# Performance work log

Hardware: AMD Instinct MI355X
Metric: run time of the kernel (lower is better)

Reference implementation:

```python
import jax, jax.numpy as jnp
import numpy as np

OBS, ACT, EMB, HID, NQ = 512, 32, 512, 512, 32
B = 32768


def setup_inputs() -> dict:
    key = jax.random.key(0)
    ks = jax.random.split(key, 12)
    s_in = 1.0 / np.sqrt(OBS + ACT)
    s_emb = 1.0 / np.sqrt(EMB)
    s_hid = 1.0 / np.sqrt(HID)
    return {
        "observation": jax.random.normal(ks[0], (B, OBS), jnp.float32),
        "prev_action": jax.random.normal(ks[1], (B, ACT), jnp.float32),
        "hidden_state": jax.random.normal(ks[2], (HID,), jnp.float32),
        "cell_state": jax.random.normal(ks[3], (HID,), jnp.float32),
        "W1": jax.random.uniform(ks[4], (EMB, OBS + ACT), jnp.float32, -s_in, s_in),
        "b1": jax.random.uniform(ks[5], (EMB,), jnp.float32, -s_in, s_in),
        "W_ih": jax.random.uniform(ks[6], (4 * HID, EMB), jnp.float32, -s_hid, s_hid),
        "b_ih": jax.random.uniform(ks[7], (4 * HID,), jnp.float32, -s_hid, s_hid),
        "W_hh": jax.random.uniform(ks[8], (4 * HID, HID), jnp.float32, -s_hid, s_hid),
        "b_hh": jax.random.uniform(ks[9], (4 * HID,), jnp.float32, -s_hid, s_hid),
        "W2": jax.random.uniform(ks[10], (NQ, HID), jnp.float32, -s_hid, s_hid),
        "b2": jax.random.uniform(ks[11], (NQ,), jnp.float32, -s_hid, s_hid),
    }


def reference(observation, prev_action, hidden_state, cell_state,
              W1, b1, W_ih, b_ih, W_hh, b_hh, W2, b2):
    # MLP1: Linear + ReLU over concat(obs, prev_action)  -> [B, EMB]
    x = jnp.concatenate([observation, prev_action], axis=-1)
    x = jax.nn.relu(x @ W1.T + b1)

    # Original torch code loops LSTMCell over batch, but reuses the SAME
    # (hidden_state, cell_state) every iteration -> fully batchable.
    # gates: [B, 4H]; h contribution is identical for all rows (broadcast).
    gates = x @ W_ih.T + b_ih + (hidden_state @ W_hh.T + b_hh)
    i, f, g, o = jnp.split(gates, 4, axis=-1)  # torch LSTMCell gate order
    i = jax.nn.sigmoid(i)
    f = jax.nn.sigmoid(f)
    g = jnp.tanh(g)
    o = jax.nn.sigmoid(o)
    c_new = f * cell_state + i * g          # [B, HID]
    h_new = o * jnp.tanh(c_new)             # [B, HID]

    q_values = h_new @ W2.T + b2             # [B, NQ]
    # torch returns last loop iteration's (h, c)
    return q_values, h_new[-1], c_new[-1]
```

## Files before the change

kernel.cpp:

```cpp
#include <hip/hip_runtime.h>
#include <stdint.h>

#define DEVINL __device__ __forceinline__

typedef __attribute__((ext_vector_type(8))) __bf16 bf16x8;
typedef __attribute__((ext_vector_type(4))) float f32x4;
typedef __attribute__((ext_vector_type(16))) float f32x16;
typedef __attribute__((ext_vector_type(4))) int i32x4;
typedef __attribute__((ext_vector_type(8))) int i32x8;

DEVINL unsigned short f2bf(float f) {
  union { float f; unsigned int u; } v; v.f = f;
  unsigned int u = v.u;
  return (unsigned short)((u + 0x7fffu + ((u >> 16) & 1u)) >> 16);
}

DEVINL unsigned char f2fp8(float f) {
  return (unsigned char)(__builtin_amdgcn_cvt_pk_fp8_f32(f, f, 0, false) & 0xff);
}

DEVINL float sigm(float x) { return __builtin_amdgcn_rcpf(1.f + __expf(-x)); }
DEVINL float tanh_(float x) {
  return 1.f - 2.f * __builtin_amdgcn_rcpf(1.f + __expf(2.f * x));
}

DEVINL size_t opt_off(int row, int k) {
  return (size_t)((row >> 5) * 8 + (k >> 6)) * 2048 + ((k >> 4) & 1) * 1024 +
         ((k >> 5) & 1) * 512 + (row & 31) * 16 + (k & 15);
}

#define GLD_LDS16(gptr, lptr)                                                  \
  __builtin_amdgcn_global_load_lds(                                            \
      (__attribute__((address_space(1))) void*)(gptr),                         \
      (__attribute__((address_space(3))) void*)(lptr), 16, 0, 0)

#define TOPBAR_4 asm volatile("s_waitcnt vmcnt(4) lgkmcnt(0)\n\ts_barrier" ::: "memory")
#define TOPBAR_1 asm volatile("s_waitcnt vmcnt(1) lgkmcnt(0)\n\ts_barrier" ::: "memory")
#define TOPBAR_0 asm volatile("s_waitcnt vmcnt(0) lgkmcnt(0)\n\ts_barrier" ::: "memory")
#define BOTBAR   asm volatile("s_waitcnt lgkmcnt(0)\n\ts_barrier" ::: "memory")

DEVINL int swz_col(int c) { return ((c & 3) ^ ((c >> 3) & 3)) * 8; }

__global__ void prep_all(const float* __restrict__ obs, const float* __restrict__ act,
                         const float* __restrict__ W1, const float* __restrict__ Wih,
                         const float* __restrict__ W2, const float* __restrict__ Whh,
                         const float* __restrict__ hid, const float* __restrict__ bhh,
                         const float* __restrict__ bih,
                         unsigned short* __restrict__ A0, unsigned short* __restrict__ W1b,
                         unsigned char* __restrict__ Wih8, unsigned short* __restrict__ W2b,
                         float* __restrict__ hvec) {
  const int bid = blockIdx.x, tid = threadIdx.x;
  if (bid < 2176) {
    const int total = 32768 * 68;
    for (int c = bid * 256 + tid; c < total; c += 2176 * 256) {
      const int b = c / 68, c8 = c % 68;
      const float* src = (c8 < 64) ? (obs + (size_t)b * 512 + c8 * 8)
                                   : (act + (size_t)b * 32 + (c8 - 64) * 8);
      float4 f0 = *(const float4*)src;
      float4 f1 = *(const float4*)(src + 4);
      unsigned short u[8] = {f2bf(f0.x), f2bf(f0.y), f2bf(f0.z), f2bf(f0.w),
                             f2bf(f1.x), f2bf(f1.y), f2bf(f1.z), f2bf(f1.w)};
      *(uint4*)(A0 + (size_t)b * 544 + c8 * 8) = *(uint4*)u;
    }
  } else if (bid < 2176 + 1312) {
    const int i = (bid - 2176) * 256 + tid;
    if (i < 69632) {
      float4 f = *(const float4*)(W1 + (size_t)i * 4);
      unsigned short u[4] = {f2bf(f.x), f2bf(f.y), f2bf(f.z), f2bf(f.w)};
      *(uint2*)(W1b + (size_t)i * 4) = *(uint2*)u;
    } else if (i < 69632 + 262144) {
      const int off = i - 69632;
      const int row = off >> 7, col0 = (off & 127) * 4;
      float4 f = *(const float4*)(Wih + (size_t)off * 4);
      int pk = __builtin_amdgcn_cvt_pk_fp8_f32(f.x * 16.f, f.y * 16.f, 0, false);
      pk = __builtin_amdgcn_cvt_pk_fp8_f32(f.z * 16.f, f.w * 16.f, pk, true);
      *(unsigned int*)(Wih8 + opt_off(row, col0)) = (unsigned int)pk;
    } else {
      const int off = i - 331776;
      float4 f = *(const float4*)(W2 + (size_t)off * 4);
      unsigned short u[4] = {f2bf(f.x), f2bf(f.y), f2bf(f.z), f2bf(f.w)};
      *(uint2*)(W2b + (size_t)off * 4) = *(uint2*)u;
    }
  } else {
    const int j = (bid - 3488) * 4 + (tid >> 6);
    const int lane = tid & 63;
    const float* w = Whh + (size_t)j * 512;
    float s = 0.f;
    for (int k = lane; k < 512; k += 64) s += w[k] * hid[k];
    for (int off = 32; off; off >>= 1) s += __shfl_down(s, off, 64);
    if (lane == 0) hvec[j] = s + bhh[j] + bih[j];
  }
}

__global__ __launch_bounds__(256, 2) void gemm1_relu(
    const unsigned short* __restrict__ A0,
    const unsigned short* __restrict__ W1b,
    const float* __restrict__ b1,
    unsigned char* __restrict__ X8) {
  constexpr int KT = 17, LD = 544;
  __shared__ __align__(16) unsigned short As[2][128 * 32];
  __shared__ __align__(16) unsigned short Bs[2][128 * 32];
  const int tid = threadIdx.x, wave = tid >> 6, lane = tid & 63;
  const int id = blockIdx.x, xcd = id & 7, slot = id >> 3;
  const int m0 = (xcd * 32 + (slot >> 2)) * 128;
  const int n0 = (slot & 3) * 128;
  const int wr = (wave >> 1) * 64, wc = (wave & 1) * 64;
  f32x4 acc[4][4] = {};

  const int c0 = tid, c1 = tid + 256;
  const unsigned short* pA0 = A0 + (size_t)(m0 + (c0 >> 2)) * LD + swz_col(c0);
  const unsigned short* pA1 = A0 + (size_t)(m0 + (c1 >> 2)) * LD + swz_col(c1);
  const unsigned short* pB0 = W1b + (size_t)(n0 + (c0 >> 2)) * LD + swz_col(c0);
  const unsigned short* pB1 = W1b + (size_t)(n0 + (c1 >> 2)) * LD + swz_col(c1);
  const int fr = lane & 15, q = lane >> 4;
  const int koff = (q ^ ((fr >> 1) & 3)) * 8;

#define STAGE1(buf)                                                            \
  do {                                                                         \
    GLD_LDS16(pA0, &As[(buf)][wave * 512]);                                    \
    GLD_LDS16(pA1, &As[(buf)][2048 + wave * 512]);                             \
    GLD_LDS16(pB0, &Bs[(buf)][wave * 512]);                                    \
    GLD_LDS16(pB1, &Bs[(buf)][2048 + wave * 512]);                             \
    pA0 += 32; pA1 += 32; pB0 += 32; pB1 += 32;                                \
  } while (0)

  STAGE1(0);
  for (int kt = 0; kt < KT; ++kt) {
    if (kt + 1 < KT) { STAGE1((kt + 1) & 1); TOPBAR_4; } else { TOPBAR_0; }
    const unsigned short* as = As[kt & 1];
    const unsigned short* bs = Bs[kt & 1];
    bf16x8 a[4], b[4];
#pragma unroll
    for (int i = 0; i < 4; ++i) a[i] = *(const bf16x8*)&as[(wr + i * 16 + fr) * 32 + koff];
#pragma unroll
    for (int j = 0; j < 4; ++j) b[j] = *(const bf16x8*)&bs[(wc + j * 16 + fr) * 32 + koff];
#pragma unroll
    for (int i = 0; i < 4; ++i)
#pragma unroll
      for (int j = 0; j < 4; ++j)
        acc[i][j] = __builtin_amdgcn_mfma_f32_16x16x32_bf16(a[i], b[j], acc[i][j], 0, 0, 0);
    BOTBAR;
  }
#undef STAGE1
  const int rbase = q * 4, cn = fr;
#pragma unroll
  for (int i = 0; i < 4; ++i)
#pragma unroll
    for (int j = 0; j < 4; ++j) {
      const int gn = n0 + wc + j * 16 + cn;
      const float bias = b1[gn];
#pragma unroll
      for (int r = 0; r < 4; ++r) {
        const int gm = m0 + wr + i * 16 + rbase + r;
        float v = acc[i][j][r] + bias;
        v = v > 0.f ? v : 0.f;
        X8[opt_off(gm, gn)] = f2fp8(v * 8.f);
      }
    }
}

__global__ __launch_bounds__(256, 2) void gemm2_lstm(
    const unsigned char* __restrict__ X8,
    const unsigned char* __restrict__ Wih8,
    const float* __restrict__ hvec,
    const float* __restrict__ cell,
    unsigned short* __restrict__ H,
    float* __restrict__ hlast,
    float* __restrict__ clast) {
  const int tid = threadIdx.x, wave = tid >> 6, lane = tid & 63;
  const int id = blockIdx.x, xcd = id & 7, slot = id >> 3;
  const int m0 = (xcd * 16 + (slot >> 4)) * 256;
  const int n0 = (slot & 15) * 32;
  const int r31 = lane & 31, g2 = lane >> 5;
  const int voff = g2 * 512 + r31 * 16;

  f32x16 acc00 = {}, acc01 = {}, acc02 = {}, acc03 = {};
  f32x16 acc10 = {}, acc11 = {}, acc12 = {}, acc13 = {};

  const unsigned char* pa0 = X8 + (size_t)((m0 >> 5) + wave * 2 + 0) * 16384 + voff;
  const unsigned char* pa1 = X8 + (size_t)((m0 >> 5) + wave * 2 + 1) * 16384 + voff;
  const unsigned char* pb0 = Wih8 + (size_t)(0 * 16 + (n0 >> 5)) * 16384 + voff;
  const unsigned char* pb1 = Wih8 + (size_t)(1 * 16 + (n0 >> 5)) * 16384 + voff;
  const unsigned char* pb2 = Wih8 + (size_t)(2 * 16 + (n0 >> 5)) * 16384 + voff;
  const unsigned char* pb3 = Wih8 + (size_t)(3 * 16 + (n0 >> 5)) * 16384 + voff;

#define LD8(dst, p)                                                            \
  do {                                                                         \
    i32x4 lo_ = *(const i32x4*)(p);                                            \
    i32x4 hi_ = *(const i32x4*)((p) + 1024);                                   \
    dst = __builtin_shufflevector(lo_, hi_, 0, 1, 2, 3, 4, 5, 6, 7);           \
  } while (0)

#define MFMA_MX(acc_, a_, b_)                                                  \
  acc_ = __builtin_amdgcn_mfma_scale_f32_32x32x64_f8f6f4(                      \
      a_, b_, acc_, 0, 0, 0, 0x7f7f7f7f, 0, 0x7f7f7f7f)

  i32x8 A0, A1;
  LD8(A0, pa0); LD8(A1, pa1);
#pragma unroll
  for (int kt = 0; kt < 8; ++kt) {
    i32x8 B0, B1, B2, B3;
    LD8(B0, pb0); LD8(B1, pb1); LD8(B2, pb2); LD8(B3, pb3);
    pb0 += 2048; pb1 += 2048; pb2 += 2048; pb3 += 2048;
    i32x8 nA0, nA1;
    if (kt < 7) {
      pa0 += 2048; pa1 += 2048;
      LD8(nA0, pa0); LD8(nA1, pa1);
    }
    MFMA_MX(acc00, A0, B0); MFMA_MX(acc01, A0, B1);
    MFMA_MX(acc02, A0, B2); MFMA_MX(acc03, A0, B3);
    MFMA_MX(acc10, A1, B0); MFMA_MX(acc11, A1, B1);
    MFMA_MX(acc12, A1, B2); MFMA_MX(acc13, A1, B3);
    if (kt < 7) { A0 = nA0; A1 = nA1; }
  }

  const int gn = n0 + r31;
  const float hv_i = hvec[gn];
  const float hv_f = hvec[gn + 512];
  const float hv_g = hvec[gn + 1024];
  const float hv_o = hvec[gn + 1536];
  const float cprev = cell[gn];
  constexpr float S = 1.f / 128.f;

#define EPILOG(F, ai, af, ag, ao)                                              \
  _Pragma("unroll")                                                            \
  for (int rg = 0; rg < 4; ++rg) {                                             \
    _Pragma("unroll")                                                          \
    for (int rr = 0; rr < 4; ++rr) {                                           \
      const int reg = rg * 4 + rr;                                             \
      const int gm = m0 + wave * 64 + (F) * 32 + rr + rg * 8 + g2 * 4;         \
      float si = sigm(ai[reg] * S + hv_i);                                     \
      float sf = sigm(af[reg] * S + hv_f);                                     \
      float tg = tanh_(ag[reg] * S + hv_g);                                    \
      float so = sigm(ao[reg] * S + hv_o);                                     \
      float cnew = sf * cprev + si * tg;                                       \
      float hnew = so * tanh_(cnew);                                           \
      H[(size_t)gm * 512 + gn] = f2bf(hnew);                                   \
      if (gm == 32767) { hlast[gn] = hnew; clast[gn] = cnew; }                 \
    }                                                                          \
  }

  EPILOG(0, acc00, acc01, acc02, acc03)
  EPILOG(1, acc10, acc11, acc12, acc13)
#undef EPILOG
#undef LD8
#undef MFMA_MX
}

__global__ __launch_bounds__(256, 2) void gemm3(
    const unsigned short* __restrict__ H,
    const unsigned short* __restrict__ W2b,
    const float* __restrict__ b2,
    float* __restrict__ Q) {
  constexpr int KT = 16, LDW = 520;
  __shared__ __align__(16) unsigned short As[2][64 * 32];
  __shared__ __align__(16) unsigned short Ws[32 * LDW];
  const int tid = threadIdx.x, wave = tid >> 6, lane = tid & 63;
  const int id = blockIdx.x;
  const int m0 = ((id & 7) * 64 + (id >> 3)) * 64;
  for (int c = tid; c < 2048; c += 256) {
    const int row = c >> 6, col8 = c & 63;
    *(uint4*)&Ws[row * LDW + col8 * 8] = *(const uint4*)(W2b + row * 512 + col8 * 8);
  }
  f32x4 acc[2] = {};
  const int c0 = tid;
  const unsigned short* pA0 = H + (size_t)(m0 + (c0 >> 2)) * 512 + swz_col(c0);
  const int fr = lane & 15, q = lane >> 4;
  const int koff = (q ^ ((fr >> 1) & 3)) * 8;

#define STAGE3(buf)                                                            \
  do {                                                                         \
    GLD_LDS16(pA0, &As[(buf)][wave * 512]);                                    \
    pA0 += 32;                                                                 \
  } while (0)

  STAGE3(0);
  for (int kt = 0; kt < KT; ++kt) {
    if (kt + 1 < KT) { STAGE3((kt + 1) & 1); TOPBAR_1; } else { TOPBAR_0; }
    const unsigned short* as = As[kt & 1];
    const int k0 = kt * 32;
    bf16x8 a  = *(const bf16x8*)&as[(wave * 16 + fr) * 32 + koff];
    bf16x8 b0 = *(const bf16x8*)&Ws[fr * LDW + k0 + q * 8];
    bf16x8 b1 = *(const bf16x8*)&Ws[(16 + fr) * LDW + k0 + q * 8];
    acc[0] = __builtin_amdgcn_mfma_f32_16x16x32_bf16(a, b0, acc[0], 0, 0, 0);
    acc[1] = __builtin_amdgcn_mfma_f32_16x16x32_bf16(a, b1, acc[1], 0, 0, 0);
    BOTBAR;
  }
#undef STAGE3
  const int rbase = q * 4;
#pragma unroll
  for (int j = 0; j < 2; ++j) {
    const int gn = j * 16 + fr;
    const float bias = b2[gn];
#pragma unroll
    for (int r = 0; r < 4; ++r) {
      const int gm = m0 + wave * 16 + rbase + r;
      Q[(size_t)gm * 32 + gn] = acc[j][r] + bias;
    }
  }
}

extern "C" void kernel_launch(void* const* d_in, const int* in_sizes, int n_in,
                              void* d_out, int out_size, void* d_ws, size_t ws_size,
                              hipStream_t stream) {
  const float* obs  = (const float*)d_in[0];
  const float* act  = (const float*)d_in[1];
  const float* hid  = (const float*)d_in[2];
  const float* cell = (const float*)d_in[3];
  const float* W1   = (const float*)d_in[4];
  const float* b1   = (const float*)d_in[5];
  const float* Wih  = (const float*)d_in[6];
  const float* bih  = (const float*)d_in[7];
  const float* Whh  = (const float*)d_in[8];
  const float* bhh  = (const float*)d_in[9];
  const float* W2   = (const float*)d_in[10];
  const float* b2   = (const float*)d_in[11];
  float* out = (float*)d_out;

  char* ws = (char*)d_ws;
  unsigned short* A0   = (unsigned short*)(ws);
  unsigned short* H    = (unsigned short*)(ws);
  unsigned char*  X8   = (unsigned char*)(ws + 35651584);
  unsigned short* W1b  = (unsigned short*)(ws + 52428800);
  unsigned char*  Wih8 = (unsigned char*)(ws + 52985856);
  unsigned short* W2b  = (unsigned short*)(ws + 54034432);
  float*          hvec = (float*)(ws + 54067200);

  prep_all<<<4000, 256, 0, stream>>>(obs, act, W1, Wih, W2, Whh, hid, bhh, bih,
                                     A0, W1b, Wih8, W2b, hvec);
  gemm1_relu<<<1024, 256, 0, stream>>>(A0, W1b, b1, X8);
  gemm2_lstm<<<2048, 256, 0, stream>>>(X8, Wih8, hvec, cell, H,
                                       out + 32768 * 32,
                                       out + 32768 * 32 + 512);
  gemm3<<<512, 256, 0, stream>>>(H, W2b, b2, out);
}
```

Before: 209.3 us.

## Stage LSTM gate weights in LDS and triple-buffer A register prefetch

The gemm2_lstm kernel now copies the block's four gate-weight tiles (64 KB) into shared memory up front with direct global-to-LDS loads, so B operands are read from LDS instead of from global memory on every k-step by every wave. The A operand prefetch becomes a three-deep register ring that loads two k-steps ahead, to hide global latency behind the MFMAs. In exchange, 64 KB of LDS per block can limit occupancy (launch bounds request two blocks per CU). Register pressure also rises from the extra A buffers.

```diff
diff --git a/kernel.cpp b/kernel.cpp
--- a/kernel.cpp
+++ b/kernel.cpp
@@ -167,6 +167,7 @@
     unsigned short* __restrict__ H,
     float* __restrict__ hlast,
     float* __restrict__ clast) {
+  __shared__ __align__(16) unsigned char Bs[4 * 16384];
   const int tid = threadIdx.x, wave = tid >> 6, lane = tid & 63;
   const int id = blockIdx.x, xcd = id & 7, slot = id >> 3;
   const int m0 = (xcd * 16 + (slot >> 4)) * 256;
@@ -174,45 +175,64 @@
   const int r31 = lane & 31, g2 = lane >> 5;
   const int voff = g2 * 512 + r31 * 16;
 
-  f32x16 acc00 = {}, acc01 = {}, acc02 = {}, acc03 = {};
-  f32x16 acc10 = {}, acc11 = {}, acc12 = {}, acc13 = {};
-
-  const unsigned char* pa0 = X8 + (size_t)((m0 >> 5) + wave * 2 + 0) * 16384 + voff;
-  const unsigned char* pa1 = X8 + (size_t)((m0 >> 5) + wave * 2 + 1) * 16384 + voff;
-  const unsigned char* pb0 = Wih8 + (size_t)(0 * 16 + (n0 >> 5)) * 16384 + voff;
-  const unsigned char* pb1 = Wih8 + (size_t)(1 * 16 + (n0 >> 5)) * 16384 + voff;
-  const unsigned char* pb2 = Wih8 + (size_t)(2 * 16 + (n0 >> 5)) * 16384 + voff;
-  const unsigned char* pb3 = Wih8 + (size_t)(3 * 16 + (n0 >> 5)) * 16384 + voff;
-
-#define LD8(dst, p)                                                            \
+  {
+    const unsigned char* bsrc =
+        Wih8 + (size_t)(wave * 16 + (n0 >> 5)) * 16384 + lane * 16;
+#pragma unroll
+    for (int s = 0; s < 16; ++s)
+      GLD_LDS16(bsrc + s * 1024, &Bs[wave * 16384 + s * 1024]);
+  }
+
+  const unsigned char* pa = X8 + (size_t)((m0 >> 5) + wave * 2) * 16384 + voff;
+  i32x8 Aa[3], Ab[3];
+#define LDA(buf, kt)                                                           \
   do {                                                                         \
-    i32x4 lo_ = *(const i32x4*)(p);                                            \
-    i32x4 hi_ = *(const i32x4*)((p) + 1024);                                   \
-    dst = __builtin_shufflevector(lo_, hi_, 0, 1, 2, 3, 4, 5, 6, 7);           \
+    i32x4 lo0 = *(const i32x4*)(pa + (kt) * 2048);                             \
+    i32x4 hi0 = *(const i32x4*)(pa + (kt) * 2048 + 1024);                      \
+    Aa[buf] = __builtin_shufflevector(lo0, hi0, 0, 1, 2, 3, 4, 5, 6, 7);       \
+    i32x4 lo1 = *(const i32x4*)(pa + 16384 + (kt) * 2048);                     \
+    i32x4 hi1 = *(const i32x4*)(pa + 16384 + (kt) * 2048 + 1024);              \
+    Ab[buf] = __builtin_shufflevector(lo1, hi1, 0, 1, 2, 3, 4, 5, 6, 7);       \
   } while (0)
 
 #define MFMA_MX(acc_, a_, b_)                                                  \
   acc_ = __builtin_amdgcn_mfma_scale_f32_32x32x64_f8f6f4(                      \
       a_, b_, acc_, 0, 0, 0, 0x7f7f7f7f, 0, 0x7f7f7f7f)
 
-  i32x8 A0, A1;
-  LD8(A0, pa0); LD8(A1, pa1);
+  LDA(0, 0);
+  LDA(1, 1);
+  __syncthreads();
+
+  f32x16 acc00 = {}, acc01 = {}, acc02 = {}, acc03 = {};
+  f32x16 acc10 = {}, acc11 = {}, acc12 = {}, acc13 = {};
+
 #pragma unroll
   for (int kt = 0; kt < 8; ++kt) {
+    const int cur = kt % 3, nx = (kt + 2) % 3;
+    if (kt < 6) LDA(nx, kt + 2);
     i32x8 B0, B1, B2, B3;
-    LD8(B0, pb0); LD8(B1, pb1); LD8(B2, pb2); LD8(B3, pb3);
-    pb0 += 2048; pb1 += 2048; pb2 += 2048; pb3 += 2048;
-    i32x8 nA0, nA1;
-    if (kt < 7) {
-      pa0 += 2048; pa1 += 2048;
-      LD8(nA0, pa0); LD8(nA1, pa1);
-    }
-    MFMA_MX(acc00, A0, B0); MFMA_MX(acc01, A0, B1);
-    MFMA_MX(acc02, A0, B2); MFMA_MX(acc03, A0, B3);
-    MFMA_MX(acc10, A1, B0); MFMA_MX(acc11, A1, B1);
-    MFMA_MX(acc12, A1, B2); MFMA_MX(acc13, A1, B3);
-    if (kt < 7) { A0 = nA0; A1 = nA1; }
-  }
+    {
+      const unsigned char* bb = &Bs[kt * 2048 + lane * 16];
+      i32x4 l0 = *(const i32x4*)(bb);
+      i32x4 h0 = *(const i32x4*)(bb + 1024);
+      i32x4 l1 = *(const i32x4*)(bb + 16384);
+      i32x4 h1 = *(const i32x4*)(bb + 16384 + 1024);
+      i32x4 l2 = *(const i32x4*)(bb + 32768);
+      i32x4 h2 = *(const i32x4*)(bb + 32768 + 1024);
+      i32x4 l3 = *(const i32x4*)(bb + 49152);
+      i32x4 h3 = *(const i32x4*)(bb + 49152 + 1024);
+      B0 = __builtin_shufflevector(l0, h0, 0, 1, 2, 3, 4, 5, 6, 7);
+      B1 = __builtin_shufflevector(l1, h1, 0, 1, 2, 3, 4, 5, 6, 7);
+      B2 = __builtin_shufflevector(l2, h2, 0, 1, 2, 3, 4, 5, 6, 7);
+      B3 = __builtin_shufflevector(l3, h3, 0, 1, 2, 3, 4, 5, 6, 7);
+    }
+    MFMA_MX(acc00, Aa[cur], B0); MFMA_MX(acc01, Aa[cur], B1);
+    MFMA_MX(acc02, Aa[cur], B2); MFMA_MX(acc03, Aa[cur], B3);
+    MFMA_MX(acc10, Ab[cur], B0); MFMA_MX(acc11, Ab[cur], B1);
+    MFMA_MX(acc12, Ab[cur], B2); MFMA_MX(acc13, Ab[cur], B3);
+  }
+#undef LDA
+#undef MFMA_MX
 
   const int gn = n0 + r31;
   const float hv_i = hvec[gn];
@@ -243,8 +263,6 @@
   EPILOG(0, acc00, acc01, acc02, acc03)
   EPILOG(1, acc10, acc11, acc12, acc13)
 #undef EPILOG
-#undef LD8
-#undef MFMA_MX
 }
 
 __global__ __launch_bounds__(256, 2) void gemm3(
```

New measurement: 205.0 us. 1.02x faster.
